# Optimization experiments

Hardware: AMD Instinct MI355X
Metric: run time of the kernel (lower is better)

Reference implementation:

```python
import jax, jax.numpy as jnp
import numpy as np
from itertools import combinations

MIN_SAMPLES = 200   # min_samples_per_class
MAX_POINTS = 64     # max_points_per_class (cap fed to VR complex)
SCALE = 1.0         # loss_scale_factor
EPS = 1e-12
N_CLASSES = 3


def setup_inputs() -> dict:
    key = jax.random.key(0)
    k1, k2, k3 = jax.random.split(key, 3)
    N, D = 120000, 768
    latent_features = jax.random.normal(k1, (N, D), dtype=jnp.float32)
    labels = jax.random.randint(k2, (N,), 0, N_CLASSES)
    # stand-in for pickled prototype H1 diagrams: [class, points, (birth, death)]
    target_diagrams = jax.random.uniform(k3, (N_CLASSES, 100, 2), dtype=jnp.float32)
    return {"latent_features": latent_features, "labels": labels,
            "target_diagrams": target_diagrams}


def _h1_pairs(Dm):
    """Exact Vietoris-Rips H1 persistence pairing (boundary-matrix reduction).
    Dm: [n,n] numpy distance matrix. Returns (birth_edges [P,2], death_edges [P,2])
    integer index arrays: birth value = Dm[bi,bj] (edge creating the cycle),
    death value = Dm[di,dj] (longest edge of the killing triangle).
    All H1 classes die in the full 2-skeleton, so no essential (inf) points."""
    n = Dm.shape[0]
    ii, jj = np.triu_indices(n, 1)
    vals = Dm[ii, jj]
    order = np.lexsort((jj, ii, vals))        # filtration order of edges
    ei, ej, ev = ii[order], jj[order], vals[order]
    m = ei.shape[0]
    rank = np.zeros((n, n), np.int64)
    rank[ei, ej] = np.arange(m)
    rank[ej, ei] = np.arange(m)
    tris = np.array(list(combinations(range(n), 3)), dtype=np.int64)  # [T,3]
    R = np.stack([rank[tris[:, 0], tris[:, 1]],
                  rank[tris[:, 0], tris[:, 2]],
                  rank[tris[:, 1], tris[:, 2]]], axis=1)              # edge ranks per tri
    maxr = R.max(axis=1)
    tval = ev[maxr]                           # triangle filtration value
    torder = np.lexsort((R[:, 0], R[:, 1], R[:, 2], maxr, tval))
    pivot_col = {}
    births, deaths = [], []
    for t in torder:
        col = set(int(r) for r in R[t])
        while col:
            piv = max(col)                    # low(column) = latest edge
            other = pivot_col.get(piv)
            if other is None:
                pivot_col[piv] = col
                births.append((ei[piv], ej[piv]))
                me = maxr[t]
                deaths.append((ei[me], ej[me]))
                break
            col ^= other                      # Z2 column addition
    if births:
        return np.asarray(births, np.int64), np.asarray(deaths, np.int64)
    return np.zeros((0, 2), np.int64), np.zeros((0, 2), np.int64)


def reference(latent_features, labels, target_diagrams):
    labels_np = np.asarray(labels)
    total = jnp.asarray(0.0, jnp.float32)
    valid = 0
    for c in range(N_CLASSES):
        idx = np.nonzero(labels_np == c)[0]
        if idx.shape[0] < MIN_SAMPLES:
            continue
        idx = idx[:MAX_POINTS]                # deterministic subsample (orig: randperm)
        pts = latent_features[jnp.asarray(idx)]              # [P, D]
        sq = jnp.sum((pts[:, None, :] - pts[None, :, :]) ** 2, axis=-1)
        Dm = jnp.sqrt(jnp.clip(sq, EPS))                     # [P, P] euclidean
        b_idx, d_idx = _h1_pairs(np.asarray(Dm))
        if b_idx.shape[0] > 0:
            tp = jnp.sum(Dm[d_idx[:, 0], d_idx[:, 1]] - Dm[b_idx[:, 0], b_idx[:, 1]])
        else:
            tp = jnp.asarray(0.0, jnp.float32)
        tgt = target_diagrams[c]
        tp_t = jnp.sum(tgt[:, 1] - tgt[:, 0])
        total = total + SCALE * (tp - tp_t) ** 2
        valid += 1
    return total / valid if valid > 0 else jnp.asarray(0.0, jnp.float32)
```

## Files before the change

### kernel.cpp

```cpp
#include <hip/hip_runtime.h>
#include <hip/hip_bf16.h>

#define NCLS 3
#define NPTS 64
#define NEDGE 2016
#define MIN_SAMP 200
#define PENDCAP 128

__device__ int          g_counts[NCLS];
__device__ int          g_sel[NCLS][NPTS];
__device__ float        g_Dm[NCLS][NPTS * NPTS];
__device__ float        g_tp[NCLS];
__device__ int          g_ovf[NCLS];
__device__ unsigned int g_rows[NCLS][NEDGE][64];

__global__ void init_k() {
    if (threadIdx.x < NCLS) { g_counts[threadIdx.x] = 0; g_ovf[threadIdx.x] = 0; }
}

__global__ __launch_bounds__(256) void count_k(const int* __restrict__ labels, int N) {
    __shared__ int c3[NCLS];
    if (threadIdx.x < NCLS) c3[threadIdx.x] = 0;
    __syncthreads();
    for (int i = blockIdx.x * blockDim.x + threadIdx.x; i < N; i += gridDim.x * blockDim.x) {
        int c = labels[i];
        if ((unsigned)c < NCLS) atomicAdd(&c3[c], 1);
    }
    __syncthreads();
    if (threadIdx.x < NCLS) atomicAdd(&g_counts[threadIdx.x], c3[threadIdx.x]);
}

__global__ __launch_bounds__(64) void select_k(const int* __restrict__ labels, int N) {
    const int lane = threadIdx.x;
    int cnt[NCLS] = {0, 0, 0};
    for (int base = 0; base < N; base += 64) {
        if (cnt[0] >= NPTS && cnt[1] >= NPTS && cnt[2] >= NPTS) break;
        int lab = (base + lane < N) ? labels[base + lane] : -1;
        for (int c = 0; c < NCLS; ++c) {
            if (cnt[c] >= NPTS) continue;
            unsigned long long m = __ballot(lab == c);
            if (!m) continue;
            int pos = cnt[c] + __popcll(m & ((1ull << lane) - 1ull));
            if (lab == c && pos < NPTS) g_sel[c][pos] = base + lane;
            cnt[c] = min(NPTS, cnt[c] + (int)__popcll(m));
        }
    }
}

__global__ __launch_bounds__(256) void dist_k(const float* __restrict__ feat) {
    int cls = blockIdx.x;
    if (g_counts[cls] < MIN_SAMP) return;
    int p = blockIdx.y * 256 + threadIdx.x;
    int i = p >> 6, j = p & 63;
    const float4* pi = (const float4*)(feat + (size_t)g_sel[cls][i] * 768);
    const float4* pj = (const float4*)(feat + (size_t)g_sel[cls][j] * 768);
    float sq = 0.f;
    #pragma unroll 4
    for (int d = 0; d < 192; ++d) {
        float4 va = pi[d], vb = pj[d];
        float dx = va.x - vb.x, dy = va.y - vb.y, dz = va.z - vb.z, dw = va.w - vb.w;
        sq = fmaf(dx, dx, sq); sq = fmaf(dy, dy, sq);
        sq = fmaf(dz, dz, sq); sq = fmaf(dw, dw, sq);
    }
    g_Dm[cls][p] = sqrtf(fmaxf(sq, 1e-12f));
}

__device__ __forceinline__ uint4 shfl4(uint4 v, int src) {
    uint4 r;
    r.x = (unsigned)__shfl((int)v.x, src);
    r.y = (unsigned)__shfl((int)v.y, src);
    r.z = (unsigned)__shfl((int)v.z, src);
    r.w = (unsigned)__shfl((int)v.w, src);
    return r;
}
__device__ __forceinline__ void xor4(uint4& a, const uint4 b) {
    a.x ^= b.x; a.y ^= b.y; a.z ^= b.z; a.w ^= b.w;
}
__device__ __forceinline__ unsigned int getw4(const uint4 a, int m) {
    return (m < 32) ? a.x : (m < 64) ? a.y : (m < 96) ? a.z : a.w;
}
__device__ __forceinline__ void set4(uint4& a, int m) {
    const unsigned int b = 1u << (m & 31);
    if (m < 32) a.x |= b; else if (m < 64) a.y |= b; else if (m < 96) a.z |= b; else a.w |= b;
}

__device__ __forceinline__ uint4 pend_apply(uint4 v, const uint4 pm,
                                            const uint4* s_pend, const unsigned char* s_pidx) {
    unsigned int w;
    w = v.x & pm.x;
    while (w) { int c = __builtin_ctz(w); w &= w - 1; xor4(v, s_pend[s_pidx[c]]); }
    w = v.y & pm.y;
    while (w) { int c = __builtin_ctz(w); w &= w - 1; xor4(v, s_pend[s_pidx[32 + c]]); }
    w = v.z & pm.z;
    while (w) { int c = __builtin_ctz(w); w &= w - 1; xor4(v, s_pend[s_pidx[64 + c]]); }
    w = v.w & pm.w;
    while (w) { int c = __builtin_ctz(w); w &= w - 1; xor4(v, s_pend[s_pidx[96 + c]]); }
    return v;
}

__global__ __launch_bounds__(1024) void persist_fast_k() {
    const int cls  = blockIdx.x;
    const int tid  = threadIdx.x;
    const int lane = tid & 63;
    const int wid  = tid >> 6;
    if (g_counts[cls] < MIN_SAMP) return;

    __shared__ union UA {
        float sDm[NPTS * NPTS];
        uint4 M[NEDGE];
    } uA;
    __shared__ short         rank2d[NPTS * NPTS];
    __shared__ unsigned char se_i[NEDGE], se_j[NEDGE];
    __shared__ float         ev[NEDGE];
    __shared__ unsigned char e2i[NEDGE], e2j[NEDGE];
    __shared__ uint4         s_pend[PENDCAP];
    __shared__ unsigned char s_pidx[128];

    for (int p = tid; p < NPTS * NPTS; p += 1024) uA.sDm[p] = g_Dm[cls][p];
    if (tid < NPTS - 1) {
        int i = tid;
        int base = i * (2 * NPTS - 1 - i) / 2;
        for (int j = i + 1; j < NPTS; ++j) {
            e2i[base + j - i - 1] = (unsigned char)i;
            e2j[base + j - i - 1] = (unsigned char)j;
        }
    }
    if (tid < NPTS) rank2d[tid * NPTS + tid] = 0x7fff;
    __syncthreads();

    for (int e = tid; e < NEDGE; e += 1024) {
        int i_ = e2i[e], j_ = e2j[e];
        float v = uA.sDm[i_ * NPTS + j_];
        int rk = 0;
        for (int f = 0; f < NEDGE; ++f) {
            int fi = e2i[f], fj = e2j[f];
            float w = uA.sDm[fi * NPTS + fj];
            bool less = (w < v) || (w == v && (fi < i_ || (fi == i_ && fj < j_)));
            rk += less ? 1 : 0;
        }
        se_i[rk] = (unsigned char)i_;
        se_j[rk] = (unsigned char)j_;
        ev[rk]   = v;
        rank2d[i_ * NPTS + j_] = (short)rk;
        rank2d[j_ * NPTS + i_] = (short)rk;
    }
    __syncthreads();

    if (wid != 0) return;

    int   rootv = lane;
    uint4 pi    = make_uint4(0u, 0u, 0u, 0u);
    uint4 occ      = make_uint4(0u, 0u, 0u, 0u);
    uint4 pendmask = make_uint4(0u, 0u, 0u, 0u);
    int   pcount = 0, inuse = 0, bail = 0;
    double birth = 0.0, death = 0.0;

    for (int r = 0; r < NEDGE; ++r) {
        if (pcount >= 64 || inuse >= 126) {
            for (int x = lane; x < r; x += 64) {
                uint4 row = uA.M[x];
                const unsigned int anyw = (row.x & pendmask.x) | (row.y & pendmask.y)
                                        | (row.z & pendmask.z) | (row.w & pendmask.w);
                if (anyw) uA.M[x] = pend_apply(row, pendmask, s_pend, s_pidx);
            }
            pi = pend_apply(pi, pendmask, s_pend, s_pidx);
            occ.x &= ~pendmask.x; occ.y &= ~pendmask.y;
            occ.z &= ~pendmask.z; occ.w &= ~pendmask.w;
            inuse -= pcount; pcount = 0;
            pendmask = make_uint4(0u, 0u, 0u, 0u);
            if (inuse >= 127) { bail = 1; break; }
        }

        const int i_ = se_i[r], j_ = se_j[r];
        const float evr = ev[r];

        const int rootI = __shfl(rootv, i_);
        const int rootJ = __shfl(rootv, j_);
        uint4 ann = shfl4(pi, i_);
        xor4(ann, shfl4(pi, j_));
        if (rootI != rootJ) {
            rootv = (rootv == rootI) ? rootJ : rootv;
        } else {
            birth += (double)evr;
            int s = (~occ.x) ? __builtin_ctz(~occ.x)
                  : (~occ.y) ? 32 + __builtin_ctz(~occ.y)
                  : (~occ.z) ? 64 + __builtin_ctz(~occ.z)
                  : (~occ.w) ? 96 + __builtin_ctz(~occ.w) : -1;
            if (s < 0) { bail = 1; break; }
            set4(occ, s); ++inuse;
            set4(ann, s);
        }
        if (lane == 0) uA.M[r] = ann;

        const int a_l = rank2d[i_ * NPTS + lane];
        const int b_l = rank2d[j_ * NPTS + lane];
        const bool validk = (lane != i_) && (lane != j_) && (a_l < r) && (b_l < r);
        if (!__ballot(validk)) continue;

        uint4 v = make_uint4(0u, 0u, 0u, 0u);
        if (validk) {
            v = uA.M[a_l];
            xor4(v, uA.M[b_l]);
            xor4(v, ann);
            v = pend_apply(v, pendmask, s_pend, s_pidx);
        }

        uint4 s4 = make_uint4(0u, 0u, 0u, 0u);
        int accidx = -1, accm = 0;
        int d = 0;
        while (true) {
            unsigned long long nzm = __ballot((v.x | v.y | v.z | v.w) != 0u);
            if (!nzm) break;
            const int l = __builtin_ctzll(nzm);
            const uint4 p = shfl4(v, l);
            const int m = p.x ? __builtin_ctz(p.x) : p.y ? 32 + __builtin_ctz(p.y)
                       : p.z ? 64 + __builtin_ctz(p.z) : 96 + __builtin_ctz(p.w);
            if (lane == l) { s4 = v; accidx = d; accm = m; }
            const unsigned int mb2 = 1u << (m & 31);
            if (getw4(v, m) & mb2) xor4(v, p);
            if (accidx >= 0 && accidx < d) {
                if (getw4(s4, m) & mb2) xor4(s4, p);
            }
            ++d;
        }
        if (d == 0) continue;
        death += (double)d * (double)evr;

        const int pbase = pcount;
        if (accidx >= 0) {
            s_pend[pbase + accidx] = s4;
            s_pidx[accm] = (unsigned char)(pbase + accidx);
        }
        for (int t = 0; t < d; ++t) {
            const unsigned long long who = __ballot(accidx == t);
            const int l = __builtin_ctzll(who);
            const int m = __shfl(accm, l);
            const uint4 u4 = shfl4(s4, l);
            set4(pendmask, m);
            const unsigned int mb2 = 1u << (m & 31);
            for (int x = lane; x < pbase; x += 64) {
                uint4 q = s_pend[x];
                if (getw4(q, m) & mb2) { xor4(q, u4); s_pend[x] = q; }
            }
        }
        pcount += d;
    }

    if (lane == 0) {
        if (bail) g_ovf[cls] = 1;
        else      g_tp[cls] = (float)(death - birth);
    }
}

__global__ __launch_bounds__(1024) void persist_exact_k() {
    const int cls  = blockIdx.x;
    const int tid  = threadIdx.x;
    const int lane = tid & 63;
    const int wid  = tid >> 6;
    if (g_counts[cls] < MIN_SAMP) return;
    if (!g_ovf[cls]) return;

    union PhaseU {
        float        sDm[NPTS * NPTS];
        unsigned int pbuf[62][64];
    };
    __shared__ PhaseU        u;
    __shared__ short         rank2d[NPTS * NPTS];
    __shared__ unsigned char e2i[NEDGE], e2j[NEDGE];
    __shared__ unsigned char se_i[NEDGE], se_j[NEDGE];
    __shared__ float         ev[NEDGE];
    __shared__ unsigned char cstate[64];
    __shared__ int           s_t;
    __shared__ double        s_birth, s_death;
    __shared__ unsigned char parent[NPTS];

    for (int p = tid; p < NPTS * NPTS; p += 1024) u.sDm[p] = g_Dm[cls][p];
    if (tid < NPTS - 1) {
        int i = tid;
        int base = i * (2 * NPTS - 1 - i) / 2;
        for (int j = i + 1; j < NPTS; ++j) {
            e2i[base + j - i - 1] = (unsigned char)i;
            e2j[base + j - i - 1] = (unsigned char)j;
        }
    }
    for (int x = tid; x < NEDGE * 64; x += 1024) {
        int rr = x >> 6, w = x & 63;
        g_rows[cls][rr][w] = (w == (rr >> 5)) ? (1u << (rr & 31)) : 0u;
    }
    if (tid < NPTS) rank2d[tid * NPTS + tid] = 0x7fff;
    __syncthreads();

    for (int e = tid; e < NEDGE; e += 1024) {
        int i_ = e2i[e], j_ = e2j[e];
        float v = u.sDm[i_ * NPTS + j_];
        int rk = 0;
        for (int f = 0; f < NEDGE; ++f) {
            int fi = e2i[f], fj = e2j[f];
            float w = u.sDm[fi * NPTS + fj];
            bool less = (w < v) || (w == v && (fi < i_ || (fi == i_ && fj < j_)));
            rk += less ? 1 : 0;
        }
        se_i[rk] = (unsigned char)i_;
        se_j[rk] = (unsigned char)j_;
        ev[rk]   = v;
        rank2d[i_ * NPTS + j_] = (short)rk;
        rank2d[j_ * NPTS + i_] = (short)rk;
    }
    __syncthreads();

    if (tid == 0) {
        for (int i = 0; i < NPTS; ++i) parent[i] = (unsigned char)i;
        double bs = 0.0;
        for (int r = 0; r < NEDGE; ++r) {
            int x = se_i[r]; while (parent[x] != x) { parent[x] = parent[parent[x]]; x = parent[x]; }
            int y = se_j[r]; while (parent[y] != y) { parent[y] = parent[parent[y]]; y = parent[y]; }
            if (x == y) bs += (double)ev[r];
            else parent[x] = (unsigned char)y;
        }
        s_birth = bs; s_death = 0.0;
    }
    __syncthreads();

    unsigned int (*Row)[64] = g_rows[cls];

    for (int r = 1; r < NEDGE; ++r) {
        const int i_ = se_i[r], j_ = se_j[r];
        const int a_l = rank2d[i_ * NPTS + lane];
        const int b_l = rank2d[j_ * NPTS + lane];
        const bool valid = (lane != i_) && (lane != j_) && (a_l < r) && (b_l < r);
        const unsigned long long mask = __ballot(valid);
        if (!mask) continue;
        const int cnt = __popcll(mask);

        {
            const unsigned int rrow = Row[r][lane];
            for (int idx = wid; idx < cnt; idx += 16) {
                unsigned long long mm = mask;
                for (int s = 0; s < idx; ++s) mm &= mm - 1;
                const int k = __builtin_ctzll(mm);
                const int a = __shfl(a_l, k);
                const int b = __shfl(b_l, k);
                const unsigned int p = Row[a][lane] ^ Row[b][lane] ^ rrow;
                u.pbuf[idx][lane] = p;
                const bool indep = (__ballot(p != 0u) != 0ull);
                if (lane == 0) cstate[idx] = indep ? 1 : 0;
            }
        }
        __syncthreads();

        while (true) {
            int c = -1;
            for (int x = 0; x < cnt; ++x) if (cstate[x] == 1) { c = x; break; }
            if (c < 0) break;
            __syncthreads();
            if (wid == 0) {
                const unsigned int pw = u.pbuf[c][lane];
                const unsigned long long m2 = __ballot(pw != 0u);
                const int fl = __builtin_ctzll(m2);
                const unsigned int w0 = (unsigned int)__shfl((int)pw, fl);
                if (lane == 0) s_t = fl * 32 + __builtin_ctz(w0);
            }
            if (tid == 0) { s_death += (double)ev[r]; cstate[c] = 2; }
            __syncthreads();
            const int t = s_t, tw = t >> 5;
            const unsigned int tb = 1u << (t & 31);
            const unsigned int pw = u.pbuf[c][lane];
            for (int rr0 = wid * 64; rr0 < NEDGE; rr0 += 1024) {
                const int rr = rr0 + lane;
                unsigned int hit = (rr < NEDGE) ? (Row[rr][tw] & tb) : 0u;
                unsigned long long mrows = __ballot(hit != 0u);
                while (mrows) {
                    const int rx = rr0 + __builtin_ctzll(mrows);
                    mrows &= mrows - 1;
                    Row[rx][lane] ^= pw;
                }
            }
            __threadfence_block();
            __syncthreads();
            {
                const unsigned int rrow2 = Row[r][lane];
                for (int idx = wid; idx < cnt; idx += 16) {
                    if (cstate[idx] != 1) continue;
                    unsigned long long mm = mask;
                    for (int s = 0; s < idx; ++s) mm &= mm - 1;
                    const int k = __builtin_ctzll(mm);
                    const int a = __shfl(a_l, k);
                    const int b = __shfl(b_l, k);
                    const unsigned int p2 = Row[a][lane] ^ Row[b][lane] ^ rrow2;
                    u.pbuf[idx][lane] = p2;
                    const bool indep = (__ballot(p2 != 0u) != 0ull);
                    if (lane == 0) cstate[idx] = indep ? 1 : 0;
                }
            }
            __syncthreads();
        }
        __syncthreads();
    }

    if (tid == 0) g_tp[cls] = (float)(s_death - s_birth);
}

__global__ void final_k(const float* __restrict__ tgt, float* __restrict__ out) {
    double total = 0.0;
    int valid = 0;
    for (int c = 0; c < NCLS; ++c) {
        if (g_counts[c] >= MIN_SAMP) {
            double tpt = 0.0;
            for (int p = 0; p < 100; ++p)
                tpt += (double)tgt[(c * 100 + p) * 2 + 1] - (double)tgt[(c * 100 + p) * 2 + 0];
            double d = (double)g_tp[c] - tpt;
            total += d * d;
            valid++;
        }
    }
    *out = valid ? (float)(total / valid) : 0.0f;
}

extern "C" void kernel_launch(void* const* d_in, const int* in_sizes, int n_in,
                              void* d_out, int out_size, void* d_ws, size_t ws_size,
                              hipStream_t stream) {
    const float* feat   = (const float*)d_in[0];
    const int*   labels = (const int*)d_in[1];
    const float* tgt    = (const float*)d_in[2];
    const int N = in_sizes[1];

    hipLaunchKernelGGL(init_k,         dim3(1),        dim3(64),   0, stream);
    hipLaunchKernelGGL(count_k,        dim3(256),      dim3(256),  0, stream, labels, N);
    hipLaunchKernelGGL(select_k,       dim3(1),        dim3(64),   0, stream, labels, N);
    hipLaunchKernelGGL(dist_k,         dim3(NCLS, 16), dim3(256),  0, stream, feat);
    hipLaunchKernelGGL(persist_fast_k, dim3(NCLS),     dim3(1024), 0, stream);
    hipLaunchKernelGGL(persist_exact_k,dim3(NCLS),     dim3(1024), 0, stream);
    hipLaunchKernelGGL(final_k,        dim3(1),        dim3(1),    0, stream, tgt, (float*)d_out);
}
```

Baseline: 2.803 ms.

## Parallelize pending-column flush across all warps and batch pending updates

Instead of exiting after setup, the other warps now stay in a barrier-driven service loop. When warp 0 flushes pending reductions into the stored matrix rows, all 16 warps apply them in parallel. The flush threshold and pending capacity are raised so flushes happen less often. The per-death serial loop that updated pending columns one at a time is replaced with a single mask-based apply, and a batched gather XOR cuts the dependency chain. The risks are block-wide barrier overhead on each flush and the correctness of the pending-update reordering.

Result: slower. 2.863 ms (+2.2%).

```diff
diff --git a/kernel.cpp b/kernel.cpp
--- a/kernel.cpp
+++ b/kernel.cpp
@@ -5,7 +5,8 @@
 #define NPTS 64
 #define NEDGE 2016
 #define MIN_SAMP 200
-#define PENDCAP 128
+#define PENDCAP 192
+#define FLUSH_PCOUNT 130
 
 __device__ int          g_counts[NCLS];
 __device__ int          g_sel[NCLS][NPTS];
@@ -98,6 +99,28 @@
     return v;
 }
 
+__device__ __forceinline__ uint4 pend_gather(uint4 v, const uint4 pm,
+                                             const uint4* s_pend, const unsigned char* s_pidx) {
+    unsigned long long wlo = (((unsigned long long)(v.y & pm.y)) << 32) | (v.x & pm.x);
+    unsigned long long whi = (((unsigned long long)(v.w & pm.w)) << 32) | (v.z & pm.z);
+    while (wlo | whi) {
+        uint4 a0 = make_uint4(0u, 0u, 0u, 0u), a1 = make_uint4(0u, 0u, 0u, 0u);
+        #pragma unroll
+        for (int t = 0; t < 8; ++t) {
+            int c0 = -1, c1 = -1;
+            if (wlo)      { c0 = __builtin_ctzll(wlo); wlo &= wlo - 1; }
+            else if (whi) { c0 = 64 + __builtin_ctzll(whi); whi &= whi - 1; }
+            if (wlo)      { c1 = __builtin_ctzll(wlo); wlo &= wlo - 1; }
+            else if (whi) { c1 = 64 + __builtin_ctzll(whi); whi &= whi - 1; }
+            if (c0 >= 0) xor4(a0, s_pend[s_pidx[c0]]);
+            if (c1 >= 0) xor4(a1, s_pend[s_pidx[c1]]);
+        }
+        xor4(a0, a1);
+        xor4(v, a0);
+    }
+    return v;
+}
+
 __global__ __launch_bounds__(1024) void persist_fast_k() {
     const int cls  = blockIdx.x;
     const int tid  = threadIdx.x;
@@ -115,6 +138,9 @@
     __shared__ unsigned char e2i[NEDGE], e2j[NEDGE];
     __shared__ uint4         s_pend[PENDCAP];
     __shared__ unsigned char s_pidx[128];
+    __shared__ uint4         s_pm;
+    __shared__ uint4         s_npm;
+    __shared__ int           s_cmd, s_flushr;
 
     for (int p = tid; p < NPTS * NPTS; p += 1024) uA.sDm[p] = g_Dm[cls][p];
     if (tid < NPTS - 1) {
@@ -146,7 +172,20 @@
     }
     __syncthreads();
 
-    if (wid != 0) return;
+    if (wid != 0) {
+        while (true) {
+            __syncthreads();
+            if (s_cmd == 2) return;
+            const uint4 pm = s_pm;
+            const int fr = s_flushr;
+            for (int x = tid; x < fr; x += 1024) {
+                uint4 row = uA.M[x];
+                if ((row.x & pm.x) | (row.y & pm.y) | (row.z & pm.z) | (row.w & pm.w))
+                    uA.M[x] = pend_gather(row, pm, s_pend, s_pidx);
+            }
+            __syncthreads();
+        }
+    }
 
     int   rootv = lane;
     uint4 pi    = make_uint4(0u, 0u, 0u, 0u);
@@ -156,14 +195,17 @@
     double birth = 0.0, death = 0.0;
 
     for (int r = 0; r < NEDGE; ++r) {
-        if (pcount >= 64 || inuse >= 126) {
-            for (int x = lane; x < r; x += 64) {
+        if (pcount >= FLUSH_PCOUNT || inuse >= 126) {
+            if (lane == 0) { s_cmd = 1; s_flushr = r; s_pm = pendmask; }
+            __syncthreads();
+            for (int x = lane; x < r; x += 1024) {
                 uint4 row = uA.M[x];
-                const unsigned int anyw = (row.x & pendmask.x) | (row.y & pendmask.y)
-                                        | (row.z & pendmask.z) | (row.w & pendmask.w);
-                if (anyw) uA.M[x] = pend_apply(row, pendmask, s_pend, s_pidx);
-            }
-            pi = pend_apply(pi, pendmask, s_pend, s_pidx);
+                if ((row.x & pendmask.x) | (row.y & pendmask.y) |
+                    (row.z & pendmask.z) | (row.w & pendmask.w))
+                    uA.M[x] = pend_gather(row, pendmask, s_pend, s_pidx);
+            }
+            __syncthreads();
+            pi = pend_gather(pi, pendmask, s_pend, s_pidx);
             occ.x &= ~pendmask.x; occ.y &= ~pendmask.y;
             occ.z &= ~pendmask.z; occ.w &= ~pendmask.w;
             inuse -= pcount; pcount = 0;
@@ -227,25 +269,25 @@
         death += (double)d * (double)evr;
 
         const int pbase = pcount;
+        if (lane < 4) ((unsigned int*)&s_npm)[lane] = 0u;
         if (accidx >= 0) {
             s_pend[pbase + accidx] = s4;
             s_pidx[accm] = (unsigned char)(pbase + accidx);
-        }
-        for (int t = 0; t < d; ++t) {
-            const unsigned long long who = __ballot(accidx == t);
-            const int l = __builtin_ctzll(who);
-            const int m = __shfl(accm, l);
-            const uint4 u4 = shfl4(s4, l);
-            set4(pendmask, m);
-            const unsigned int mb2 = 1u << (m & 31);
-            for (int x = lane; x < pbase; x += 64) {
-                uint4 q = s_pend[x];
-                if (getw4(q, m) & mb2) { xor4(q, u4); s_pend[x] = q; }
-            }
+            atomicOr(&((unsigned int*)&s_npm)[accm >> 5], 1u << (accm & 31));
+        }
+        const uint4 npm = s_npm;
+        pendmask.x |= npm.x; pendmask.y |= npm.y;
+        pendmask.z |= npm.z; pendmask.w |= npm.w;
+        for (int x = lane; x < pbase; x += 64) {
+            uint4 q = s_pend[x];
+            if ((q.x & npm.x) | (q.y & npm.y) | (q.z & npm.z) | (q.w & npm.w))
+                s_pend[x] = pend_apply(q, npm, s_pend, s_pidx);
         }
         pcount += d;
     }
 
+    if (lane == 0) s_cmd = 2;
+    __syncthreads();
     if (lane == 0) {
         if (bail) g_ovf[cls] = 1;
         else      g_tp[cls] = (float)(death - birth);
```

## Prefetch next edge data, index pending rows by pivot, batch pending updates

Applied to the files above, without the earlier changes.

Software-pipelines the per-edge reduction loop by loading the next edge's endpoints, value, neighbor ranks and matrix rows during the current iteration. Pending reduced rows are now stored directly by pivot index, which removes the indirection table. Updates to existing pending rows are batched with a single mask per step instead of one pass per new pivot. The flush now triggers only on annotation slot pressure, not on pending count, so flushes happen less often. The cost is more register pressure and reloading of prefetched rows after a flush.

Result: slower. 3.217 ms (+14.8%).

```diff
diff --git a/kernel.cpp b/kernel.cpp
--- a/kernel.cpp
+++ b/kernel.cpp
@@ -5,7 +5,6 @@
 #define NPTS 64
 #define NEDGE 2016
 #define MIN_SAMP 200
-#define PENDCAP 128
 
 __device__ int          g_counts[NCLS];
 __device__ int          g_sel[NCLS][NPTS];
@@ -83,18 +82,20 @@
     const unsigned int b = 1u << (m & 31);
     if (m < 32) a.x |= b; else if (m < 64) a.y |= b; else if (m < 96) a.z |= b; else a.w |= b;
 }
-
-__device__ __forceinline__ uint4 pend_apply(uint4 v, const uint4 pm,
-                                            const uint4* s_pend, const unsigned char* s_pidx) {
+__device__ __forceinline__ bool any4(const uint4 a, const uint4 b) {
+    return ((a.x & b.x) | (a.y & b.y) | (a.z & b.z) | (a.w & b.w)) != 0u;
+}
+
+__device__ __forceinline__ uint4 pend_apply(uint4 v, const uint4 pm, const uint4* pend) {
     unsigned int w;
     w = v.x & pm.x;
-    while (w) { int c = __builtin_ctz(w); w &= w - 1; xor4(v, s_pend[s_pidx[c]]); }
+    while (w) { int c = __builtin_ctz(w); w &= w - 1; xor4(v, pend[c]); }
     w = v.y & pm.y;
-    while (w) { int c = __builtin_ctz(w); w &= w - 1; xor4(v, s_pend[s_pidx[32 + c]]); }
+    while (w) { int c = __builtin_ctz(w); w &= w - 1; xor4(v, pend[32 + c]); }
     w = v.z & pm.z;
-    while (w) { int c = __builtin_ctz(w); w &= w - 1; xor4(v, s_pend[s_pidx[64 + c]]); }
+    while (w) { int c = __builtin_ctz(w); w &= w - 1; xor4(v, pend[64 + c]); }
     w = v.w & pm.w;
-    while (w) { int c = __builtin_ctz(w); w &= w - 1; xor4(v, s_pend[s_pidx[96 + c]]); }
+    while (w) { int c = __builtin_ctz(w); w &= w - 1; xor4(v, pend[96 + c]); }
     return v;
 }
 
@@ -113,8 +114,8 @@
     __shared__ unsigned char se_i[NEDGE], se_j[NEDGE];
     __shared__ float         ev[NEDGE];
     __shared__ unsigned char e2i[NEDGE], e2j[NEDGE];
-    __shared__ uint4         s_pend[PENDCAP];
-    __shared__ unsigned char s_pidx[128];
+    __shared__ uint4         s_pend[128];
+    __shared__ unsigned char s_plist[128];
 
     for (int p = tid; p < NPTS * NPTS; p += 1024) uA.sDm[p] = g_Dm[cls][p];
     if (tid < NPTS - 1) {
@@ -152,27 +153,37 @@
     uint4 pi    = make_uint4(0u, 0u, 0u, 0u);
     uint4 occ      = make_uint4(0u, 0u, 0u, 0u);
     uint4 pendmask = make_uint4(0u, 0u, 0u, 0u);
-    int   pcount = 0, inuse = 0, bail = 0;
+    int   pcount = 0, inuse = 0, plc = 0, bail = 0;
     double birth = 0.0, death = 0.0;
 
+    int   pf_i = se_i[0], pf_j = se_j[0];
+    float pf_e = ev[0];
+    short pf_a = rank2d[pf_i * NPTS + lane];
+    short pf_b = rank2d[pf_j * NPTS + lane];
+    bool  pf_v = false;
+    uint4 pf_Ma = make_uint4(0u, 0u, 0u, 0u), pf_Mb = pf_Ma;
+
     for (int r = 0; r < NEDGE; ++r) {
-        if (pcount >= 64 || inuse >= 126) {
+        const int   i_  = pf_i, j_ = pf_j;
+        const float evr = pf_e;
+        const short a_l = pf_a, b_l = pf_b;
+        const bool  validk = pf_v;
+        uint4 Ma = pf_Ma, Mb = pf_Mb;
+
+        if (inuse >= 126) {
             for (int x = lane; x < r; x += 64) {
                 uint4 row = uA.M[x];
-                const unsigned int anyw = (row.x & pendmask.x) | (row.y & pendmask.y)
-                                        | (row.z & pendmask.z) | (row.w & pendmask.w);
-                if (anyw) uA.M[x] = pend_apply(row, pendmask, s_pend, s_pidx);
-            }
-            pi = pend_apply(pi, pendmask, s_pend, s_pidx);
+                if (any4(row, pendmask)) uA.M[x] = pend_apply(row, pendmask, s_pend);
+            }
+            pi = pend_apply(pi, pendmask, s_pend);
             occ.x &= ~pendmask.x; occ.y &= ~pendmask.y;
             occ.z &= ~pendmask.z; occ.w &= ~pendmask.w;
-            inuse -= pcount; pcount = 0;
+            inuse -= pcount; pcount = 0; plc = 0;
             pendmask = make_uint4(0u, 0u, 0u, 0u);
-            if (inuse >= 127) { bail = 1; break; }
-        }
-
-        const int i_ = se_i[r], j_ = se_j[r];
-        const float evr = ev[r];
+            if (inuse >= 126) { bail = 1; break; }
+            Ma = uA.M[validk ? (int)a_l : 0];
+            Mb = uA.M[validk ? (int)b_l : 0];
+        }
 
         const int rootI = __shfl(rootv, i_);
         const int rootJ = __shfl(rootv, j_);
@@ -192,17 +203,25 @@
         }
         if (lane == 0) uA.M[r] = ann;
 
-        const int a_l = rank2d[i_ * NPTS + lane];
-        const int b_l = rank2d[j_ * NPTS + lane];
-        const bool validk = (lane != i_) && (lane != j_) && (a_l < r) && (b_l < r);
+        {
+            const int rn = (r + 1 < NEDGE) ? r + 1 : r;
+            pf_i = se_i[rn]; pf_j = se_j[rn];
+            pf_e = ev[rn];
+            pf_a = rank2d[pf_i * NPTS + lane];
+            pf_b = rank2d[pf_j * NPTS + lane];
+            pf_v = (lane != pf_i) && (lane != pf_j) && (pf_a < rn) && (pf_b < rn);
+            pf_Ma = uA.M[pf_v ? (int)pf_a : 0];
+            pf_Mb = uA.M[pf_v ? (int)pf_b : 0];
+        }
+
         if (!__ballot(validk)) continue;
 
         uint4 v = make_uint4(0u, 0u, 0u, 0u);
         if (validk) {
-            v = uA.M[a_l];
-            xor4(v, uA.M[b_l]);
+            v = Ma;
+            xor4(v, Mb);
             xor4(v, ann);
-            v = pend_apply(v, pendmask, s_pend, s_pidx);
+            v = pend_apply(v, pendmask, s_pend);
         }
 
         uint4 s4 = make_uint4(0u, 0u, 0u, 0u);
@@ -226,24 +245,25 @@
         if (d == 0) continue;
         death += (double)d * (double)evr;
 
-        const int pbase = pcount;
         if (accidx >= 0) {
-            s_pend[pbase + accidx] = s4;
-            s_pidx[accm] = (unsigned char)(pbase + accidx);
-        }
+            s_pend[accm] = s4;
+            s_plist[plc + accidx] = (unsigned char)accm;
+        }
+        uint4 npm = make_uint4(0u, 0u, 0u, 0u);
         for (int t = 0; t < d; ++t) {
             const unsigned long long who = __ballot(accidx == t);
             const int l = __builtin_ctzll(who);
             const int m = __shfl(accm, l);
-            const uint4 u4 = shfl4(s4, l);
-            set4(pendmask, m);
-            const unsigned int mb2 = 1u << (m & 31);
-            for (int x = lane; x < pbase; x += 64) {
-                uint4 q = s_pend[x];
-                if (getw4(q, m) & mb2) { xor4(q, u4); s_pend[x] = q; }
-            }
-        }
-        pcount += d;
+            set4(npm, m);
+        }
+        for (int x = lane; x < plc; x += 64) {
+            const int p = s_plist[x];
+            uint4 q = s_pend[p];
+            if (any4(q, npm)) s_pend[p] = pend_apply(q, npm, s_pend);
+        }
+        plc += d; pcount += d;
+        pendmask.x |= npm.x; pendmask.y |= npm.y;
+        pendmask.z |= npm.z; pendmask.w |= npm.w;
     }
 
     if (lane == 0) {
```
